# Kernel optimization log

Hardware: AMD Instinct MI355X
Metric: run time of the kernel (lower is better)

Reference implementation:

```python
import jax, jax.numpy as jnp
import numpy as np

K = 16
CIN = 128
COUT = 128
EPS = 1e-5
SLOPE = 0.01  # default negative_slope of nn.LeakyReLU


def _bn(w, gamma, beta):
    # BatchNorm1d in training mode over channel axis (last): stats over (N, k)
    mean = jnp.mean(w, axis=(0, 1))
    var = jnp.var(w, axis=(0, 1))  # biased variance, as torch uses for normalization
    return (w - mean) * jax.lax.rsqrt(var + EPS) * gamma + beta


def _leaky(x):
    return jnp.where(x >= 0, x, SLOPE * x)


def setup_inputs() -> dict:
    key = jax.random.key(0)
    ks = jax.random.split(key, 10)
    N = 8192
    s = 0.05
    return {
        "fea_i": jax.random.normal(ks[0], (N, CIN), jnp.float32),
        "fea_last": jax.random.normal(ks[1], (N, CIN), jnp.float32),
        "xyz_i": jax.random.uniform(ks[2], (N, 3), jnp.float32),
        "xyz_last": jax.random.uniform(ks[3], (N, 3), jnp.float32),
        "batch": jnp.zeros((N,), jnp.int32),
        "Wq": jax.random.normal(ks[4], (COUT, CIN), jnp.float32) * s,
        "bq": jnp.zeros((COUT,), jnp.float32),
        "Wk": jax.random.normal(ks[5], (COUT, CIN), jnp.float32) * s,
        "bk": jnp.zeros((COUT,), jnp.float32),
        "Wv": jax.random.normal(ks[6], (COUT, CIN), jnp.float32) * s,
        "bv": jnp.zeros((COUT,), jnp.float32),
        "bn1_gamma": jnp.ones((COUT,), jnp.float32),
        "bn1_beta": jnp.zeros((COUT,), jnp.float32),
        "Wl": jax.random.normal(ks[7], (COUT, COUT), jnp.float32) * s,
        "bl": jnp.zeros((COUT,), jnp.float32),
        "bn2_gamma": jnp.ones((COUT,), jnp.float32),
        "bn2_beta": jnp.zeros((COUT,), jnp.float32),
    }


def reference(fea_i, fea_last, xyz_i, xyz_last, batch, Wq, bq, Wk, bk, Wv, bv,
              bn1_gamma, bn1_beta, Wl, bl, bn2_gamma, bn2_beta):
    # knn: for each point in xyz_last, K nearest neighbors in xyz_i (single batch)
    d2 = jnp.sum((xyz_last[:, None, :] - xyz_i[None, :, :]) ** 2, axis=-1)  # (N, N)
    _, idx = jax.lax.top_k(-d2, K)  # (N, K) indices into xyz_i / fea_i

    fk = fea_i[idx]                                   # (N, K, CIN) gathered neighbor feats
    q = fea_last @ Wq.T + bq                          # (N, COUT); fea_last[idx_last] == row-repeat
    kk = jnp.einsum('nkc,oc->nko', fk, Wk) + bk       # (N, K, COUT)
    w = q[:, None, :] - kk                            # (N, K, COUT)

    # lin_w: BN -> LeakyReLU -> Linear -> BN -> LeakyReLU
    w = _leaky(_bn(w, bn1_gamma, bn1_beta))
    w = jnp.einsum('nko,po->nkp', w, Wl) + bl
    w = _leaky(_bn(w, bn2_gamma, bn2_beta))

    w = jax.nn.softmax(w, axis=1)                     # softmax over K neighbors
    v = jnp.einsum('nkc,oc->nko', fk, Wv) + bv        # (N, K, COUT)
    return jnp.sum(w * v, axis=1)                     # (N, COUT)
```

## Files before the change

### kernel.cpp

```cpp
#include <hip/hip_runtime.h>
#include <stdint.h>

#define NPTS   8192
#define NROWS  (NPTS * 16)
#define SLOPE  0.01f
#define BN_EPS 1e-5f

#define TP     0.13f
#define TP2    (TP * TP)
#define CAP    152
#define TF     0.2f
#define TF2    0.04f
#define CAPF   408
#define EPSB   1e-5f

#define OFF_Q      0u
#define OFF_KP     4194304u
#define OFF_VP     8388608u
#define OFF_STATS  12582912u
#define OFF_TAB    12845056u
#define OFF_IDX    13041664u
#define OFF_BIG    13585408u
#define WS_NEED    47139840u

#define T_PCNT 0
#define T_POFF 512
#define T_PCUR 1025

typedef __bf16 bf16x8 __attribute__((ext_vector_type(8)));
typedef float  f32x4  __attribute__((ext_vector_type(4)));

__device__ __forceinline__ unsigned int pack_bf2(float lo, float hi) {
  unsigned int a = __float_as_uint(lo);
  unsigned int b = __float_as_uint(hi);
  unsigned int ra = (a + 0x7fffu + ((a >> 16) & 1u)) >> 16;
  unsigned int rb = (b + 0x7fffu + ((b >> 16) & 1u)) & 0xffff0000u;
  return ra | rb;
}
__device__ __forceinline__ unsigned short bf1(float v) {
  unsigned int a = __float_as_uint(v);
  return (unsigned short)((a + 0x7fffu + ((a >> 16) & 1u)) >> 16);
}
__device__ __forceinline__ float bf2f(unsigned short u) {
  return __uint_as_float(((unsigned int)u) << 16);
}

__device__ __forceinline__ int cell_of(float x, float y, float z) {
  int cx = min(7, max(0, (int)(x * 8.f)));
  int cy = min(7, max(0, (int)(y * 8.f)));
  int cz = min(7, max(0, (int)(z * 8.f)));
  return (cz * 8 + cy) * 8 + cx;
}

__device__ __forceinline__ void insert16(unsigned long long* key, unsigned long long kk) {
  if (kk < key[15]) {
    #pragma unroll
    for (int u = 15; u >= 1; --u) {
      bool cm1 = kk < key[u - 1];
      bool cs  = kk < key[u];
      key[u] = cm1 ? key[u - 1] : (cs ? kk : key[u]);
    }
    key[0] = (kk < key[0]) ? kk : key[0];
  }
}

template<int D>
__device__ __forceinline__ void extract_topk(const unsigned long long* __restrict__ poolq, int n, int lane,
                                             int* __restrict__ sidxq, int* __restrict__ idxoq) {
  unsigned long long lst[D];
  #pragma unroll
  for (int j = 0; j < D; ++j) lst[j] = ~0ull;
  for (int j = lane; j < n; j += 64) {
    unsigned long long kk = poolq[j];
    #pragma unroll
    for (int u = D - 1; u >= 1; --u) {
      bool cm1 = kk < lst[u - 1];
      bool cs  = kk < lst[u];
      lst[u] = cm1 ? lst[u - 1] : (cs ? kk : lst[u]);
    }
    lst[0] = (kk < lst[0]) ? kk : lst[0];
  }
  int myidx = 0;
  #pragma unroll 1
  for (int r = 0; r < 16; ++r) {
    const float hd = __uint_as_float((unsigned int)(lst[0] >> 32));
    float wm = hd;
    #pragma unroll
    for (int o = 32; o; o >>= 1) wm = fminf(wm, __shfl_xor(wm, o));
    bool iswin = (hd == wm);
    const unsigned long long wmask = __ballot(iswin);
    unsigned int widx;
    if (__popcll(wmask) > 1) {
      unsigned int mi = iswin ? (unsigned int)lst[0] : 0xffffffffu;
      #pragma unroll
      for (int o = 32; o; o >>= 1) {
        unsigned int u = (unsigned int)__shfl_xor((int)mi, o);
        mi = (u < mi) ? u : mi;
      }
      widx = mi;
      iswin = iswin && ((unsigned int)lst[0] == mi);
    } else {
      const int wl = (int)__builtin_ctzll(wmask);
      widx = (unsigned int)__builtin_amdgcn_readlane((int)(unsigned int)lst[0], wl);
    }
    #pragma unroll
    for (int u = 0; u < D - 1; ++u) lst[u] = iswin ? lst[u + 1] : lst[u];
    lst[D - 1] = iswin ? ~0ull : lst[D - 1];
    if (lane == r) myidx = (int)widx;
  }
  if (lane < 16) { idxoq[lane] = myidx; sidxq[lane] = myidx; }
}

__device__ __forceinline__ int scan_ball(const int* __restrict__ poff, const float4* __restrict__ bp,
                                         float qx, float qy, float qz, float rad, float r2, int cap,
                                         unsigned long long* __restrict__ poolw,
                                         int lane, unsigned long long below) {
  const int lx = max(0, (int)floorf((qx - rad - EPSB) * 8.f));
  const int hx = min(7, (int)floorf((qx + rad + EPSB) * 8.f));
  const int ly = max(0, (int)floorf((qy - rad - EPSB) * 8.f));
  const int hy = min(7, (int)floorf((qy + rad + EPSB) * 8.f));
  const int lz = max(0, (int)floorf((qz - rad - EPSB) * 8.f));
  const int hz = min(7, (int)floorf((qz + rad + EPSB) * 8.f));
  const int nrY = hy - ly + 1, nrows = nrY * (hz - lz + 1);
  int zi = 0;
  #pragma unroll
  for (int z2 = 1; z2 < 5; ++z2) zi += (lane >= z2 * nrY) ? 1 : 0;
  const int yi = lane - zi * nrY;
  int rs = 0, re = 0;
  if (lane < nrows) {
    const int crow = ((lz + zi) * 8 + (ly + yi)) * 8;
    rs = poff[crow + lx]; re = poff[crow + hx + 1];
  }
  int cnt = 0;
  for (int r = 0; r < nrows; ++r) {
    const int rsr = __builtin_amdgcn_readlane(rs, r);
    const int rer = __builtin_amdgcn_readlane(re, r);
    for (int base = rsr; base < rer; base += 64) {
      const int pos = base + lane;
      const float4 pp = bp[pos];
      float dx = qx - pp.x, dy = qy - pp.y, dz = qz - pp.z;
      float dd = fmaf(dx, dx, fmaf(dy, dy, dz * dz));
      bool g = (pos < rer) && (dd < r2);
      unsigned long long mask = __ballot(g);
      int p2 = cnt + (int)__popcll(mask & below);
      if (g && p2 < cap)
        poolw[p2] = ((unsigned long long)__float_as_uint(dd) << 32) | (unsigned int)__float_as_int(pp.w);
      cnt += (int)__popcll(mask);
    }
  }
  return cnt;
}

__global__ __launch_bounds__(256) void k_zero(int* __restrict__ tab,
                                              float* __restrict__ stats,
                                              float4* __restrict__ bp) {
  const int T = blockIdx.x * 256 + threadIdx.x;
  if (T < 8192) stats[T] = 0.f;
  if (T < 512)  tab[T_PCNT + T] = 0;
  if (T < 64)   bp[NPTS + T] = make_float4(1e9f, 1e9f, 1e9f, __int_as_float(0));
}

__global__ __launch_bounds__(256) void k_count(const float* __restrict__ xyz_i,
                                               int* __restrict__ tab) {
  const int t = blockIdx.x * 256 + threadIdx.x;
  atomicAdd(&tab[T_PCNT + cell_of(xyz_i[t * 3], xyz_i[t * 3 + 1], xyz_i[t * 3 + 2])], 1);
}

__global__ __launch_bounds__(512) void k_offsets(int* __restrict__ tab) {
  __shared__ int ls[512];
  const int t = threadIdx.x;
  const int v = tab[T_PCNT + t];
  ls[t] = v;
  __syncthreads();
  for (int ofs = 1; ofs < 512; ofs <<= 1) {
    int add = (t >= ofs) ? ls[t - ofs] : 0;
    __syncthreads();
    ls[t] += add;
    __syncthreads();
  }
  tab[T_POFF + t] = ls[t] - v;
  tab[T_PCUR + t] = ls[t] - v;
  if (t == 511) tab[T_POFF + 512] = ls[511];
}

__global__ __launch_bounds__(256) void k_scatter(const float* __restrict__ xyz_i,
                                                 int* __restrict__ tab,
                                                 float4* __restrict__ bp) {
  const int t = blockIdx.x * 256 + threadIdx.x;
  float x = xyz_i[t * 3], y = xyz_i[t * 3 + 1], z = xyz_i[t * 3 + 2];
  int pos = atomicAdd(&tab[T_PCUR + cell_of(x, y, z)], 1);
  bp[pos] = make_float4(x, y, z, __int_as_float(t));
}

__global__ __launch_bounds__(256) void k_proj(const float* __restrict__ fea_i,
                                              const float* __restrict__ fea_last,
                                              const float* __restrict__ Wq,
                                              const float* __restrict__ Wk,
                                              const float* __restrict__ Wv,
                                              const float* __restrict__ bq,
                                              const float* __restrict__ bk,
                                              const float* __restrict__ bv,
                                              float* __restrict__ Qo,
                                              float* __restrict__ Kpo,
                                              float* __restrict__ Vpo) {
  const int z = blockIdx.y;
  const float* A    = (z == 0) ? fea_last : fea_i;
  const float* W    = (z == 0) ? Wq : ((z == 1) ? Wk : Wv);
  const float* bias = (z == 0) ? bq : ((z == 1) ? bk : bv);
  float* Out        = (z == 0) ? Qo : ((z == 1) ? Kpo : Vpo);

  __shared__ unsigned short wl[128 * 128];
  const int t = threadIdx.x;
  const int lane = t & 63, w = t >> 6;

  #pragma unroll
  for (int i = 0; i < 8; ++i) {
    const int chunk = i * 256 + t;
    const int p = chunk >> 4, cseg = chunk & 15;
    const float4 wa = *(const float4*)(W + (size_t)p * 128 + cseg * 8);
    const float4 wb = *(const float4*)(W + (size_t)p * 128 + cseg * 8 + 4);
    uint4 pk;
    pk.x = pack_bf2(wa.x, wa.y); pk.y = pack_bf2(wa.z, wa.w);
    pk.z = pack_bf2(wb.x, wb.y); pk.w = pack_bf2(wb.z, wb.w);
    *(uint4*)((char*)wl + p * 256 + ((cseg * 16) ^ ((p & 7) << 4))) = pk;
  }
  __syncthreads();

  const int rowtile = blockIdx.x * 64 + w * 16;
  const int kslot = lane & 15, kgrp = lane >> 4;
  const float* Arow = A + (size_t)(rowtile + kslot) * 128;

  f32x4 acc[8];
  #pragma unroll
  for (int tt = 0; tt < 8; ++tt) acc[tt] = (f32x4){0.f, 0.f, 0.f, 0.f};

  #pragma unroll
  for (int s = 0; s < 4; ++s) {
    const int c0 = s * 32 + kgrp * 8;
    const float4 qa = *(const float4*)(Arow + c0);
    const float4 qb = *(const float4*)(Arow + c0 + 4);
    uint4 af;
    af.x = pack_bf2(qa.x, qa.y); af.y = pack_bf2(qa.z, qa.w);
    af.z = pack_bf2(qb.x, qb.y); af.w = pack_bf2(qb.z, qb.w);
    const bf16x8 Af = __builtin_bit_cast(bf16x8, af);
    const int cbyte = s * 64 + kgrp * 16;
    #pragma unroll
    for (int tt = 0; tt < 8; ++tt) {
      const int prow = tt * 16 + kslot;
      const uint4 bw = *(const uint4*)((const char*)wl + prow * 256 + (cbyte ^ ((prow & 7) << 4)));
      acc[tt] = __builtin_amdgcn_mfma_f32_16x16x32_bf16(Af, __builtin_bit_cast(bf16x8, bw), acc[tt], 0, 0, 0);
    }
  }

  #pragma unroll
  for (int tt = 0; tt < 8; ++tt) {
    const int col = tt * 16 + kslot;
    const float bb = bias[col];
    #pragma unroll
    for (int r = 0; r < 4; ++r) {
      const int row = rowtile + kgrp * 4 + r;
      Out[(size_t)row * 128 + col] = acc[tt][r] + bb;
    }
  }
}

__global__ __launch_bounds__(256) void k_knn(const int* __restrict__ tab,
                                             const float4* __restrict__ bp,
                                             const float* __restrict__ xyz_last,
                                             const float* __restrict__ Q,
                                             const float* __restrict__ Kp,
                                             int* __restrict__ idxo,
                                             float* __restrict__ st1) {
  __shared__ unsigned long long pool[4][CAPF];
  __shared__ int sidx[4][16];
  const int t = threadIdx.x, lane = t & 63, wave = t >> 6;
  const int q = blockIdx.x * 4 + wave;
  const float qx = xyz_last[q * 3];
  const float qy = xyz_last[q * 3 + 1];
  const float qz = xyz_last[q * 3 + 2];
  const int* poff = &tab[T_POFF];
  const unsigned long long below = (1ull << lane) - 1ull;

  int cnt = scan_ball(poff, bp, qx, qy, qz, TP, TP2, CAP, &pool[wave][0], lane, below);
  if (cnt >= 16 && cnt <= CAP) {
    extract_topk<3>(&pool[wave][0], cnt, lane, &sidx[wave][0], &idxo[q * 16]);
  } else {
    cnt = scan_ball(poff, bp, qx, qy, qz, TF, TF2, CAPF, &pool[wave][0], lane, below);
    if (cnt >= 16 && cnt <= CAPF) {
      extract_topk<7>(&pool[wave][0], cnt, lane, &sidx[wave][0], &idxo[q * 16]);
    } else {
      unsigned long long key[16];
      #pragma unroll
      for (int u = 0; u < 16; ++u) key[u] = ~0ull;
      for (int it = 0; it < NPTS / 64; ++it) {
        const float4 pp = bp[it * 64 + lane];
        float dx = qx - pp.x, dy = qy - pp.y, dz = qz - pp.z;
        float dd = fmaf(dx, dx, fmaf(dy, dy, dz * dz));
        insert16(key, ((unsigned long long)__float_as_uint(dd) << 32) | (unsigned int)__float_as_int(pp.w));
      }
      unsigned long long myout = ~0ull;
      #pragma unroll 1
      for (int r = 0; r < 16; ++r) {
        unsigned long long w = key[0];
        #pragma unroll
        for (int o = 32; o; o >>= 1) {
          unsigned long long u = __shfl_xor(w, o);
          w = (u < w) ? u : w;
        }
        if (key[0] == w) {
          #pragma unroll
          for (int u = 0; u < 15; ++u) key[u] = key[u + 1];
          key[15] = ~0ull;
        }
        if (lane == r) myout = w;
      }
      if (lane < 16) {
        idxo[q * 16 + lane] = (int)(myout & 0xffffffffull);
        sidx[wave][lane] = (int)(myout & 0xffffffffull);
      }
    }
  }

  const int c0 = lane * 2;
  const float2 qv = *(const float2*)(Q + (size_t)q * 128 + c0);
  float s0 = 0.f, s1 = 0.f, v0 = 0.f, v1 = 0.f;
  #pragma unroll 4
  for (int k = 0; k < 16; ++k) {
    const int pid = sidx[wave][k];
    const float2 kv = *(const float2*)(Kp + (size_t)pid * 128 + c0);
    const float w0 = qv.x - kv.x, w1 = qv.y - kv.y;
    s0 += w0; v0 += w0 * w0;
    s1 += w1; v1 += w1 * w1;
  }
  const int slot = (blockIdx.x & 15) * 256;
  atomicAdd(&st1[slot + c0],       s0);
  atomicAdd(&st1[slot + c0 + 1],   s1);
  atomicAdd(&st1[slot + 128 + c0], v0);
  atomicAdd(&st1[slot + 129 + c0], v1);
}

__global__ void k_bnfin(const float* __restrict__ stats, int nrep, float invM,
                        const float* __restrict__ gamma, const float* __restrict__ beta,
                        float* __restrict__ bn) {
  const int o = threadIdx.x;
  float s = 0.f, q = 0.f;
  for (int r = 0; r < nrep; ++r) { s += stats[r * 256 + o]; q += stats[r * 256 + 128 + o]; }
  float mean = s * invM;
  float var  = fmaf(-mean, mean, q * invM);
  float sc = gamma[o] * rsqrtf(var + BN_EPS);
  bn[o]       = sc;
  bn[128 + o] = fmaf(-mean, sc, beta[o]);
}

__global__ __launch_bounds__(256) void k_mid(const float* __restrict__ Q,
                                             const float* __restrict__ Kp,
                                             const int* __restrict__ idx,
                                             const float* __restrict__ Wl,
                                             const float* __restrict__ bl,
                                             const float* __restrict__ bn1,
                                             float* __restrict__ stats2,
                                             unsigned short* __restrict__ Y) {
  __shared__ union {
    unsigned short wl[128 * 128];
    struct {
      unsigned short stage[64][136];
      float red[4 * 256];
    } ep;
  } sm;

  const int t = threadIdx.x;
  const int lane = t & 63, w = t >> 6;
  const int rowbase = blockIdx.x * 64;

  #pragma unroll
  for (int i = 0; i < 8; ++i) {
    const int chunk = i * 256 + t;
    const int p = chunk >> 4, cseg = chunk & 15;
    const float4 wa = *(const float4*)(Wl + (size_t)p * 128 + cseg * 8);
    const float4 wb = *(const float4*)(Wl + (size_t)p * 128 + cseg * 8 + 4);
    uint4 pk;
    pk.x = pack_bf2(wa.x, wa.y); pk.y = pack_bf2(wa.z, wa.w);
    pk.z = pack_bf2(wb.x, wb.y); pk.w = pack_bf2(wb.z, wb.w);
    *(uint4*)((char*)sm.wl + p * 256 + ((cseg * 16) ^ ((p & 7) << 4))) = pk;
  }
  __syncthreads();

  const int n = blockIdx.x * 4 + w;
  const int kslot = lane & 15;
  const int kgrp  = lane >> 4;
  const int pid = idx[n * 16 + kslot];
  const float* Qrow = Q + (size_t)n * 128;
  const float* Krow = Kp + (size_t)pid * 128;

  f32x4 acc[8];
  #pragma unroll
  for (int tt = 0; tt < 8; ++tt) acc[tt] = (f32x4){0.f, 0.f, 0.f, 0.f};

  #pragma unroll
  for (int s = 0; s < 4; ++s) {
    const int c0 = s * 32 + kgrp * 8;
    const float4 qa = *(const float4*)(Qrow + c0);
    const float4 qb = *(const float4*)(Qrow + c0 + 4);
    const float4 ka = *(const float4*)(Krow + c0);
    const float4 kb = *(const float4*)(Krow + c0 + 4);
    const float4 sa = *(const float4*)(bn1 + c0);
    const float4 sb = *(const float4*)(bn1 + c0 + 4);
    const float4 ha = *(const float4*)(bn1 + 128 + c0);
    const float4 hb = *(const float4*)(bn1 + 128 + c0 + 4);
    float x[8];
    x[0] = fmaf(qa.x - ka.x, sa.x, ha.x);
    x[1] = fmaf(qa.y - ka.y, sa.y, ha.y);
    x[2] = fmaf(qa.z - ka.z, sa.z, ha.z);
    x[3] = fmaf(qa.w - ka.w, sa.w, ha.w);
    x[4] = fmaf(qb.x - kb.x, sb.x, hb.x);
    x[5] = fmaf(qb.y - kb.y, sb.y, hb.y);
    x[6] = fmaf(qb.z - kb.z, sb.z, hb.z);
    x[7] = fmaf(qb.w - kb.w, sb.w, hb.w);
    uint4 af;
    af.x = pack_bf2(fmaxf(x[0], SLOPE * x[0]), fmaxf(x[1], SLOPE * x[1]));
    af.y = pack_bf2(fmaxf(x[2], SLOPE * x[2]), fmaxf(x[3], SLOPE * x[3]));
    af.z = pack_bf2(fmaxf(x[4], SLOPE * x[4]), fmaxf(x[5], SLOPE * x[5]));
    af.w = pack_bf2(fmaxf(x[6], SLOPE * x[6]), fmaxf(x[7], SLOPE * x[7]));
    const bf16x8 A = __builtin_bit_cast(bf16x8, af);
    const int cbyte = s * 64 + kgrp * 16;
    #pragma unroll
    for (int tt = 0; tt < 8; ++tt) {
      const int prow = tt * 16 + kslot;
      const uint4 bw = *(const uint4*)((const char*)sm.wl + prow * 256 + (cbyte ^ ((prow & 7) << 4)));
      acc[tt] = __builtin_amdgcn_mfma_f32_16x16x32_bf16(A, __builtin_bit_cast(bf16x8, bw), acc[tt], 0, 0, 0);
    }
  }
  __syncthreads();

  #pragma unroll
  for (int tt = 0; tt < 8; ++tt) {
    const int col = tt * 16 + kslot;
    const float bb = bl[col];
    float s = 0.f, q2 = 0.f;
    #pragma unroll
    for (int r = 0; r < 4; ++r) {
      const float v = acc[tt][r] + bb;
      s += v; q2 += v * v;
      sm.ep.stage[w * 16 + kgrp * 4 + r][col] = bf1(v);
    }
    s  += __shfl_xor(s, 16);  s  += __shfl_xor(s, 32);
    q2 += __shfl_xor(q2, 16); q2 += __shfl_xor(q2, 32);
    if (kgrp == 0) {
      sm.ep.red[w * 256 + col]       = s;
      sm.ep.red[w * 256 + 128 + col] = q2;
    }
  }
  __syncthreads();

  #pragma unroll
  for (int i = 0; i < 4; ++i) {
    const int chunk = i * 256 + t;
    const int row = chunk >> 4, cc = chunk & 15;
    const uint4 v = *(const uint4*)&sm.ep.stage[row][cc * 8];
    *(uint4*)&Y[(size_t)(rowbase + row) * 128 + cc * 8] = v;
  }
  {
    const float tot = sm.ep.red[t] + sm.ep.red[256 + t] + sm.ep.red[512 + t] + sm.ep.red[768 + t];
    atomicAdd(&stats2[(blockIdx.x & 15) * 256 + t], tot);
  }
}

__global__ __launch_bounds__(128) void k_epi(const unsigned short* __restrict__ Y,
                                             const float* __restrict__ Vp,
                                             const int* __restrict__ idx,
                                             const float* __restrict__ bn2,
                                             float* __restrict__ out) {
  const int n = blockIdx.x;
  const int p = threadIdx.x;
  const float s2 = bn2[p], sh2 = bn2[128 + p];
  float z[16];
  #pragma unroll
  for (int k = 0; k < 16; ++k) {
    float yv = bf2f(Y[(size_t)(n * 16 + k) * 128 + p]);
    float v = fmaf(yv, s2, sh2);
    z[k] = (v >= 0.f) ? v : SLOPE * v;
  }
  float m = z[0];
  #pragma unroll
  for (int k = 1; k < 16; ++k) m = fmaxf(m, z[k]);
  float acc = 0.f, denom = 0.f;
  #pragma unroll
  for (int k = 0; k < 16; ++k) {
    float e = __expf(z[k] - m);
    denom += e;
    const int pid = idx[n * 16 + k];
    acc = fmaf(e, Vp[(size_t)pid * 128 + p], acc);
  }
  out[(size_t)n * 128 + p] = acc / denom;
}

extern "C" void kernel_launch(void* const* d_in, const int* in_sizes, int n_in,
                              void* d_out, int out_size, void* d_ws, size_t ws_size,
                              hipStream_t stream) {
  const float* fea_i    = (const float*)d_in[0];
  const float* fea_last = (const float*)d_in[1];
  const float* xyz_i    = (const float*)d_in[2];
  const float* xyz_last = (const float*)d_in[3];
  const float* Wq = (const float*)d_in[5];
  const float* bq = (const float*)d_in[6];
  const float* Wk = (const float*)d_in[7];
  const float* bk = (const float*)d_in[8];
  const float* Wv = (const float*)d_in[9];
  const float* bv = (const float*)d_in[10];
  const float* g1 = (const float*)d_in[11];
  const float* b1 = (const float*)d_in[12];
  const float* Wl = (const float*)d_in[13];
  const float* bl = (const float*)d_in[14];
  const float* g2 = (const float*)d_in[15];
  const float* b2 = (const float*)d_in[16];

  if (ws_size < (size_t)WS_NEED) return;

  char* ws = (char*)d_ws;
  float*  Q      = (float*)(ws + OFF_Q);
  float*  Kp     = (float*)(ws + OFF_KP);
  float*  Vp     = (float*)(ws + OFF_VP);
  int*    tab    = (int*)  (ws + OFF_TAB);
  int*    idxb   = (int*)  (ws + OFF_IDX);
  float*  st1    = (float*)(ws + OFF_STATS);
  float*  st2    = st1 + 4096;
  float*  bn1    = st1 + 8192;
  float*  bn2    = st1 + 8448;
  float4* bp     = (float4*)(ws + OFF_BIG);
  unsigned short* Y = (unsigned short*)(ws + OFF_BIG);

  k_zero<<<33, 256, 0, stream>>>(tab, st1, bp);
  k_proj<<<dim3(128, 3), 256, 0, stream>>>(fea_i, fea_last, Wq, Wk, Wv, bq, bk, bv, Q, Kp, Vp);
  k_count<<<32, 256, 0, stream>>>(xyz_i, tab);
  k_offsets<<<1, 512, 0, stream>>>(tab);
  k_scatter<<<32, 256, 0, stream>>>(xyz_i, tab, bp);
  k_knn<<<2048, 256, 0, stream>>>(tab, bp, xyz_last, Q, Kp, idxb, st1);
  k_bnfin<<<1, 128, 0, stream>>>(st1, 16, 1.f / (float)NROWS, g1, b1, bn1);
  k_mid<<<2048, 256, 0, stream>>>(Q, Kp, idxb, Wl, bl, bn1, st2, Y);
  k_bnfin<<<1, 128, 0, stream>>>(st2, 16, 1.f / (float)NROWS, g2, b2, bn2);
  k_epi<<<8192, 128, 0, stream>>>(Y, Vp, idxb, bn2, (float*)d_out);
}
```

Before: 126.5 us.

## Use per-lane candidate slots for first kNN ball and block-reduce BN stats

The first-radius ball scan now stores in-radius candidates into small per-lane LDS slots (depth 6) instead of compacting them into a shared pool with ballot prefix sums. Each lane then keeps a local sorted list, and a tournament selects the top 16. If any lane overflows or the total is under 16, it falls back to the wider ball scan. The BN1 statistic atomics are also reduced across the four waves in shared memory first, cutting global atomics by a factor of four at the cost of a block barrier.

Measured after the change: 116.9 us. 1.08x faster.

```diff
diff --git a/kernel.cpp b/kernel.cpp
--- a/kernel.cpp
+++ b/kernel.cpp
@@ -8,7 +8,8 @@
 
 #define TP     0.13f
 #define TP2    (TP * TP)
-#define CAP    152
+#define LDEP   6
+#define LSTR   7
 #define TF     0.2f
 #define TF2    0.04f
 #define CAPF   408
@@ -65,21 +66,8 @@
 }
 
 template<int D>
-__device__ __forceinline__ void extract_topk(const unsigned long long* __restrict__ poolq, int n, int lane,
+__device__ __forceinline__ void tournament16(unsigned long long (&lst)[D], int lane,
                                              int* __restrict__ sidxq, int* __restrict__ idxoq) {
-  unsigned long long lst[D];
-  #pragma unroll
-  for (int j = 0; j < D; ++j) lst[j] = ~0ull;
-  for (int j = lane; j < n; j += 64) {
-    unsigned long long kk = poolq[j];
-    #pragma unroll
-    for (int u = D - 1; u >= 1; --u) {
-      bool cm1 = kk < lst[u - 1];
-      bool cs  = kk < lst[u];
-      lst[u] = cm1 ? lst[u - 1] : (cs ? kk : lst[u]);
-    }
-    lst[0] = (kk < lst[0]) ? kk : lst[0];
-  }
   int myidx = 0;
   #pragma unroll 1
   for (int r = 0; r < 16; ++r) {
@@ -111,6 +99,25 @@
   if (lane < 16) { idxoq[lane] = myidx; sidxq[lane] = myidx; }
 }
 
+template<int D>
+__device__ __forceinline__ void extract_topk(const unsigned long long* __restrict__ poolq, int n, int lane,
+                                             int* __restrict__ sidxq, int* __restrict__ idxoq) {
+  unsigned long long lst[D];
+  #pragma unroll
+  for (int j = 0; j < D; ++j) lst[j] = ~0ull;
+  for (int j = lane; j < n; j += 64) {
+    unsigned long long kk = poolq[j];
+    #pragma unroll
+    for (int u = D - 1; u >= 1; --u) {
+      bool cm1 = kk < lst[u - 1];
+      bool cs  = kk < lst[u];
+      lst[u] = cm1 ? lst[u - 1] : (cs ? kk : lst[u]);
+    }
+    lst[0] = (kk < lst[0]) ? kk : lst[0];
+  }
+  tournament16<D>(lst, lane, sidxq, idxoq);
+}
+
 __device__ __forceinline__ int scan_ball(const int* __restrict__ poff, const float4* __restrict__ bp,
                                          float qx, float qy, float qz, float rad, float r2, int cap,
                                          unsigned long long* __restrict__ poolw,
@@ -271,8 +278,9 @@
                                              const float* __restrict__ Kp,
                                              int* __restrict__ idxo,
                                              float* __restrict__ st1) {
-  __shared__ unsigned long long pool[4][CAPF];
+  __shared__ unsigned long long pool[4][64 * LSTR];
   __shared__ int sidx[4][16];
+  __shared__ float red[4][256];
   const int t = threadIdx.x, lane = t & 63, wave = t >> 6;
   const int q = blockIdx.x * 4 + wave;
   const float qx = xyz_last[q * 3];
@@ -281,13 +289,67 @@
   const int* poff = &tab[T_POFF];
   const unsigned long long below = (1ull << lane) - 1ull;
 
-  int cnt = scan_ball(poff, bp, qx, qy, qz, TP, TP2, CAP, &pool[wave][0], lane, below);
-  if (cnt >= 16 && cnt <= CAP) {
-    extract_topk<3>(&pool[wave][0], cnt, lane, &sidx[wave][0], &idxo[q * 16]);
+  unsigned long long* myslots = &pool[wave][lane * LSTR];
+  int cnt = 0;
+  {
+    const int lx = max(0, (int)floorf((qx - TP - EPSB) * 8.f));
+    const int hx = min(7, (int)floorf((qx + TP + EPSB) * 8.f));
+    const int ly = max(0, (int)floorf((qy - TP - EPSB) * 8.f));
+    const int hy = min(7, (int)floorf((qy + TP + EPSB) * 8.f));
+    const int lz = max(0, (int)floorf((qz - TP - EPSB) * 8.f));
+    const int hz = min(7, (int)floorf((qz + TP + EPSB) * 8.f));
+    const int nrY = hy - ly + 1, nrows = nrY * (hz - lz + 1);
+    int zi = 0;
+    #pragma unroll
+    for (int z2 = 1; z2 < 5; ++z2) zi += (lane >= z2 * nrY) ? 1 : 0;
+    const int yi = lane - zi * nrY;
+    int rs = 0, re = 0;
+    if (lane < nrows) {
+      const int crow = ((lz + zi) * 8 + (ly + yi)) * 8;
+      rs = poff[crow + lx]; re = poff[crow + hx + 1];
+    }
+    for (int r = 0; r < nrows; ++r) {
+      const int rsr = __builtin_amdgcn_readlane(rs, r);
+      const int rer = __builtin_amdgcn_readlane(re, r);
+      #pragma unroll 2
+      for (int base = rsr; base < rer; base += 64) {
+        const int pos = base + lane;
+        const float4 pp = bp[pos];
+        float dx = qx - pp.x, dy = qy - pp.y, dz = qz - pp.z;
+        float dd = fmaf(dx, dx, fmaf(dy, dy, dz * dz));
+        if ((pos < rer) && (dd < TP2)) {
+          if (cnt < LDEP)
+            myslots[cnt] = ((unsigned long long)__float_as_uint(dd) << 32) | (unsigned int)__float_as_int(pp.w);
+          ++cnt;
+        }
+      }
+    }
+  }
+  const bool anyover = __ballot(cnt > LDEP) != 0ull;
+  int tot = cnt;
+  #pragma unroll
+  for (int o = 32; o; o >>= 1) tot += __shfl_xor(tot, o);
+
+  if (!anyover && tot >= 16) {
+    unsigned long long lst[LDEP];
+    #pragma unroll
+    for (int j = 0; j < LDEP; ++j) lst[j] = ~0ull;
+    for (int j = 0; j < cnt; ++j) {
+      unsigned long long kk = myslots[j];
+      #pragma unroll
+      for (int u = LDEP - 1; u >= 1; --u) {
+        bool cm1 = kk < lst[u - 1];
+        bool cs  = kk < lst[u];
+        lst[u] = cm1 ? lst[u - 1] : (cs ? kk : lst[u]);
+      }
+      lst[0] = (kk < lst[0]) ? kk : lst[0];
+    }
+    tournament16<LDEP>(lst, lane, &sidx[wave][0], &idxo[q * 16]);
   } else {
-    cnt = scan_ball(poff, bp, qx, qy, qz, TF, TF2, CAPF, &pool[wave][0], lane, below);
-    if (cnt >= 16 && cnt <= CAPF) {
-      extract_topk<7>(&pool[wave][0], cnt, lane, &sidx[wave][0], &idxo[q * 16]);
+    unsigned long long* flat = &pool[wave][0];
+    int c1 = scan_ball(poff, bp, qx, qy, qz, TF, TF2, CAPF, flat, lane, below);
+    if (c1 >= 16 && c1 <= CAPF) {
+      extract_topk<7>(flat, c1, lane, &sidx[wave][0], &idxo[q * 16]);
     } else {
       unsigned long long key[16];
       #pragma unroll
@@ -332,11 +394,13 @@
     s0 += w0; v0 += w0 * w0;
     s1 += w1; v1 += w1 * w1;
   }
-  const int slot = (blockIdx.x & 15) * 256;
-  atomicAdd(&st1[slot + c0],       s0);
-  atomicAdd(&st1[slot + c0 + 1],   s1);
-  atomicAdd(&st1[slot + 128 + c0], v0);
-  atomicAdd(&st1[slot + 129 + c0], v1);
+  red[wave][c0]       = s0;  red[wave][c0 + 1]   = s1;
+  red[wave][128 + c0] = v0;  red[wave][129 + c0] = v1;
+  __syncthreads();
+  {
+    const float totv = red[0][t & 255] + red[1][t & 255] + red[2][t & 255] + red[3][t & 255];
+    atomicAdd(&st1[(blockIdx.x & 15) * 256 + (t & 255)], totv);
+  }
 }
 
 __global__ void k_bnfin(const float* __restrict__ stats, int nrep, float invM,
```
